# Kernel tuning notes

Measured on AMD Instinct MI355X. Metric: run time of the kernel, lower is better.

Reference implementation:

```python
import jax, jax.numpy as jnp
import numpy as np
import math

# dims (match init_kwargs / input_specs)
T, B, S = 2048, 8, 512
D, H, DFF, NQ, W = 512, 8, 2048, 10, 16
EPS = 1e-5
NEG = -1e30


def _ln(x, g, b):
    mu = jnp.mean(x, axis=-1, keepdims=True)
    var = jnp.mean((x - mu) ** 2, axis=-1, keepdims=True)
    return (x - mu) * jax.lax.rsqrt(var + EPS) * g + b


def setup_inputs() -> dict:
    key = jax.random.key(0)
    ks = jax.random.split(key, 10)
    f = lambda k, shape, s=0.02: jax.random.normal(k, shape, jnp.float32) * s
    return {
        'tgt': jax.random.normal(ks[0], (T, B, D), jnp.float32),
        'memory': jax.random.normal(ks[1], (S, B, D), jnp.float32),
        'queries': f(ks[2], (NQ, D), 1.0 / math.sqrt(D)),
        'wk': f(ks[3], (NQ, 1), 1.0 / math.sqrt(NQ)),
        'in_proj_w': f(ks[4], (3 * D, D)),
        'in_proj_b': jnp.zeros((3 * D,), jnp.float32),
        'out_proj_w': f(ks[5], (D, D)),
        'out_proj_b': jnp.zeros((D,), jnp.float32),
        'lin1_w': f(ks[6], (DFF, D)),
        'lin1_b': jnp.zeros((DFF,), jnp.float32),
        'lin2_w': f(ks[7], (D, DFF)),
        'lin2_b': jnp.zeros((D,), jnp.float32),
        'ln1_g': jnp.ones((D,), jnp.float32), 'ln1_b': jnp.zeros((D,), jnp.float32),
        'ln2_g': jnp.ones((D,), jnp.float32), 'ln2_b': jnp.zeros((D,), jnp.float32),
        'ln3_g': jnp.ones((D,), jnp.float32), 'ln3_b': jnp.zeros((D,), jnp.float32),
    }


def _qa_block(x, queries, wk):
    # x: (T, B, D). Learned queries: per-head unit-norm + depth scale (QaN).
    dh = D // H
    q = queries.reshape(NQ, H, dh)
    q = q / (jnp.linalg.norm(q, axis=-1, keepdims=True) + 1e-6)
    q = (q / math.sqrt(dh)).reshape(NQ, D)
    # LocalAttention(window=W, look_backward=1, look_forward=1, non-causal, autopad)
    # k = v = x; T % W == 0 so autopad is a no-op.
    xb = jnp.transpose(x, (1, 0, 2))                       # (B, T, D)
    nw = T // W
    scale = D ** -0.5                                      # dim_head = D (single-head local attn)
    bk = xb.reshape(B, nw, W, D)
    pad = jnp.zeros((B, 1, W, D), x.dtype)
    bkp = jnp.concatenate([pad, bk, pad], axis=1)          # (B, nw+2, W, D)
    kv = jnp.concatenate([bkp[:, i:i + nw] for i in range(3)], axis=2)  # (B, nw, 3W, D)
    win_ok = jnp.pad(jnp.ones((nw,), bool), (1, 1))
    vm = jnp.stack([win_ok[i:i + nw] for i in range(3)], axis=1)        # (nw, 3)
    kmask = jnp.repeat(vm, W, axis=1)                                   # (nw, 3W)
    # The query vector is identical for every time step, so every position in a
    # window sees the same (query, keyset) pair -> one attention row per (n, window).
    sim = jnp.einsum('nd,bmjd->bnmj', q * scale, kv)       # (B, NQ, nw, 3W)
    sim = jnp.where(kmask[None, None], sim, NEG)
    attn = jax.nn.softmax(sim, axis=-1)
    out = jnp.einsum('bnmj,bmjd->bnmd', attn, kv)          # (B, NQ, nw, D)
    out = jnp.einsum('bnmd,n->bmd', out, wk[:, 0])         # mix N queries via wk (N,1)
    out = jnp.broadcast_to(out[:, :, None], (B, nw, W, D)).reshape(B, T, D)
    return jnp.transpose(out, (1, 0, 2))                   # (T, B, D)


def _mha_block(x, mem, in_w, in_b, out_w, out_b):
    dh = D // H
    wq, wkk, wv = jnp.split(in_w, 3, axis=0)
    bq, bk, bv = jnp.split(in_b, 3)
    q = (x @ wq.T + bq).reshape(T, B, H, dh).transpose(1, 2, 0, 3)   # (B,H,T,dh)
    k = (mem @ wkk.T + bk).reshape(S, B, H, dh).transpose(1, 2, 0, 3)
    v = (mem @ wv.T + bv).reshape(S, B, H, dh).transpose(1, 2, 0, 3)
    attn = jax.nn.softmax(jnp.einsum('bhtd,bhsd->bhts', q, k) / math.sqrt(dh), axis=-1)
    o = jnp.einsum('bhts,bhsd->bhtd', attn, v).transpose(2, 0, 1, 3).reshape(T, B, D)
    return o @ out_w.T + out_b


def reference(tgt, memory, queries, wk, in_proj_w, in_proj_b, out_proj_w, out_proj_b,
              lin1_w, lin1_b, lin2_w, lin2_b, ln1_g, ln1_b, ln2_g, ln2_b, ln3_g, ln3_b):
    # post-norm (norm_first=False), eval mode: dropouts + stochastic_depth(rate=0) are identity
    x = tgt
    x = _ln(x + _qa_block(x, queries, wk), ln1_g, ln1_b)
    x = _ln(x + _mha_block(x, memory, in_proj_w, in_proj_b, out_proj_w, out_proj_b), ln2_g, ln2_b)
    ff = jax.nn.relu(x @ lin1_w.T + lin1_b) @ lin2_w.T + lin2_b
    x = _ln(x + ff, ln3_g, ln3_b)
    # x = tgt + stochastic_depth(x - tgt) == x in eval / rate 0
    return x
```

## Files before the change

kernel.cpp:

```cpp
#include <hip/hip_runtime.h>


typedef unsigned short u16;
typedef unsigned int u32;
typedef short short8_t __attribute__((ext_vector_type(8)));
typedef float f32x4 __attribute__((ext_vector_type(4)));

#define TT 2048
#define BB 8
#define SS 512
#define DD 512
#define HH 8
#define DH 64
#define DFF 2048
#define NQ 10
#define WW 16
#define NW 128
#define KVPART 2097152

__device__ __forceinline__ float b2f(u16 u) {
    return __uint_as_float(((unsigned int)u) << 16);
}
__device__ __forceinline__ u16 f2b(float f) {
    unsigned int x = __float_as_uint(f);
    unsigned int r = x + 0x7FFFu + ((x >> 16) & 1u);
    return (u16)(r >> 16);
}
__device__ __forceinline__ u32 cvt_pk_bf16(float lo, float hi) {
    u32 r;
    asm volatile("v_cvt_pk_bf16_f32 %0, %1, %2" : "=v"(r) : "v"(lo), "v"(hi));
    return r;
}
__device__ __forceinline__ float wave_sum(float v) {
    #pragma unroll
    for (int o = 32; o > 0; o >>= 1) v += __shfl_xor(v, o, 64);
    return v;
}
__device__ __forceinline__ float wave_max(float v) {
    #pragma unroll
    for (int o = 32; o > 0; o >>= 1) v = fmaxf(v, __shfl_xor(v, o, 64));
    return v;
}
__device__ __forceinline__ void load4(const u16* p, float* v) {
    ushort4 t = *(const ushort4*)p;
    v[0] = b2f(t.x); v[1] = b2f(t.y); v[2] = b2f(t.z); v[3] = b2f(t.w);
}
__device__ __forceinline__ void load4(const float* p, float* v) {
    float4 t = *(const float4*)p;
    v[0] = t.x; v[1] = t.y; v[2] = t.z; v[3] = t.w;
}
__device__ __forceinline__ void st1(u16* p, float v) { *p = f2b(v); }
__device__ __forceinline__ void st1(float* p, float v) { *p = v; }

__device__ __forceinline__ void async16(const u16* g, u16* l) {
    __builtin_amdgcn_global_load_lds((const __attribute__((address_space(1))) u32*)g,
                                     (__attribute__((address_space(3))) u32*)l, 16, 0, 0);
}

__device__ __forceinline__ void xcd_remap(int& bx, int& by) {
    int flat = blockIdx.y * gridDim.x + blockIdx.x;
    int xcd = flat & 7;
    int j = flat >> 3;
    by = xcd * ((int)gridDim.y >> 3) + j / (int)gridDim.x;
    bx = j % (int)gridDim.x;
}

__device__ __forceinline__ void cvt_block(const float* s, u16* d, int base) {
    int i = base + threadIdx.x * 4;
    float4 v = *(const float4*)(s + i);
    ushort4 o;
    o.x = f2b(v.x); o.y = f2b(v.y); o.z = f2b(v.z); o.w = f2b(v.w);
    *(ushort4*)(d + i) = o;
}

__global__ __launch_bounds__(256) void cvt2_kernel(const float* __restrict__ s0,
                                                   const float* __restrict__ s1,
                                                   u16* __restrict__ d0,
                                                   u16* __restrict__ d1) {
    int bid = blockIdx.x;
    if (bid < 2048) cvt_block(s0, d0, bid * 1024);
    else            cvt_block(s1, d1, (bid - 2048) * 1024);
}

__global__ __launch_bounds__(256) void cvt3_kernel(const float* __restrict__ s0,
                                                   const float* __restrict__ s1,
                                                   const float* __restrict__ s2,
                                                   u16* __restrict__ d0,
                                                   u16* __restrict__ d1,
                                                   u16* __restrict__ d2) {
    int bid = blockIdx.x;
    if (bid < 256) {
        cvt_block(s0, d0, bid * 1024);
    } else if (bid < 1280) {
        cvt_block(s1, d1, (bid - 256) * 1024);
    } else {
        int g = (bid - 1280) * 256 + threadIdx.x;
        int l = g & 63, ot = (g >> 6) & 31, c = g >> 11;
        int quad = l >> 4;
        int o = ot * 16 + (l & 15);
        const float* src = s2 + (size_t)o * DFF + c * 32 + 4 * quad;
        float4 v0 = *(const float4*)(src);
        float4 v1 = *(const float4*)(src + 16);
        ushort4 o0, o1;
        o0.x = f2b(v0.x); o0.y = f2b(v0.y); o0.z = f2b(v0.z); o0.w = f2b(v0.w);
        o1.x = f2b(v1.x); o1.y = f2b(v1.y); o1.z = f2b(v1.z); o1.w = f2b(v1.w);
        u16* dst = d2 + (size_t)g * 8;
        *(ushort4*)(dst) = o0;
        *(ushort4*)(dst + 4) = o1;
    }
}

__global__ __launch_bounds__(512) void qeff_kernel(const float* __restrict__ queries,
                                                   float* __restrict__ qeff) {
    int d = threadIdx.x;
    const float KS = 0.0055242717280199026f;
    for (int n = 0; n < NQ; n++) {
        float v = queries[n * DD + d];
        float ss = wave_sum(v * v);
        float norm = sqrtf(ss);
        qeff[n * DD + d] = v / (norm + 1e-6f) * KS;
    }
}

__global__ __launch_bounds__(256) void p_kernel(const float* __restrict__ x,
                                                const float* __restrict__ qeff,
                                                float* __restrict__ p) {
    __shared__ float qe[NQ * DD];
    for (int i = threadIdx.x; i < NQ * DD; i += 256) qe[i] = qeff[i];
    __syncthreads();
    int b = blockIdx.x >> 9;
    int t = ((blockIdx.x & 511) << 2) + (threadIdx.x >> 6);
    int lane = threadIdx.x & 63;
    const float* xr = x + ((size_t)t * BB + b) * DD;
    float acc[NQ];
    #pragma unroll
    for (int n = 0; n < NQ; n++) acc[n] = 0.f;
    #pragma unroll
    for (int c = 0; c < 8; c++) {
        int d = c * 64 + lane;
        float xv = xr[d];
        #pragma unroll
        for (int n = 0; n < NQ; n++) acc[n] += xv * qe[n * DD + d];
    }
    #pragma unroll
    for (int n = 0; n < NQ; n++) {
        float s = wave_sum(acc[n]);
        if (lane == 0) p[((size_t)(b * NQ + n)) * TT + t] = s;
    }
}

__global__ __launch_bounds__(256) void winmix_kernel(const float* __restrict__ p,
                                                     const float* __restrict__ wk,
                                                     const float* __restrict__ x,
                                                     float* __restrict__ mixed) {
    __shared__ float As[48];
    int id = blockIdx.x;
    int b = id >> 7, m = id & 127;
    if (threadIdx.x < 64) {
        int j = threadIdx.x;
        int tj = (m - 1) * WW + j;
        bool valid = (j < 48) && (tj >= 0) && (tj < TT);
        float acc = 0.f;
        for (int n = 0; n < NQ; n++) {
            float v = valid ? p[((size_t)(b * NQ + n)) * TT + tj] : -1e30f;
            float mx = wave_max(v);
            float e = valid ? __expf(v - mx) : 0.f;
            float s = wave_sum(e);
            acc += wk[n] * (e / s);
        }
        if (j < 48) As[j] = acc;
    }
    __syncthreads();
    int d0 = threadIdx.x, d1 = threadIdx.x + 256;
    float a0 = 0.f, a1 = 0.f;
    int tb = (m - 1) * WW;
    for (int j = 0; j < 48; j++) {
        int t = tb + j;
        if ((unsigned)t < (unsigned)TT) {
            float aj = As[j];
            const float* xr = x + ((size_t)t * BB + b) * DD;
            a0 += aj * xr[d0];
            a1 += aj * xr[d1];
        }
    }
    mixed[(size_t)id * DD + d0] = a0;
    mixed[(size_t)id * DD + d1] = a1;
}

__global__ __launch_bounds__(256) void ln_qa_kernel(const float* __restrict__ a,
                                                    const float* __restrict__ mixed,
                                                    const float* __restrict__ g,
                                                    const float* __restrict__ bt,
                                                    u16* __restrict__ out) {
    int r = blockIdx.x * 4 + (threadIdx.x >> 6);
    int lane = threadIdx.x & 63;
    int t = r >> 3, b = r & 7;
    const float* ar = a + (size_t)r * DD;
    const float* mr = mixed + ((size_t)(b * NW + (t >> 4))) * DD;
    int d0 = lane * 8;
    float av[8], mv[8], gg[8], bb[8];
    load4(ar + d0, av); load4(ar + d0 + 4, av + 4);
    load4(mr + d0, mv); load4(mr + d0 + 4, mv + 4);
    load4(g + d0, gg);  load4(g + d0 + 4, gg + 4);
    load4(bt + d0, bb); load4(bt + d0 + 4, bb + 4);
    float v[8];
    float s = 0.f, s2 = 0.f;
    #pragma unroll
    for (int u = 0; u < 8; u++) { v[u] = av[u] + mv[u]; s += v[u]; s2 += v[u] * v[u]; }
    s = wave_sum(s); s2 = wave_sum(s2);
    float mu = s * (1.f / DD);
    float var = s2 * (1.f / DD) - mu * mu;
    float rs = rsqrtf(var + 1e-5f);
    #pragma unroll
    for (int u = 0; u < 8; u++) out[(size_t)r * DD + d0 + u] = f2b((v[u] - mu) * rs * gg[u] + bb[u]);
}

template <typename OT>
__global__ __launch_bounds__(256) void ln_rows_kernel(const u16* __restrict__ a,
                                                      const u16* __restrict__ bsrc,
                                                      const float* __restrict__ g,
                                                      const float* __restrict__ bt,
                                                      OT* __restrict__ out) {
    int r = blockIdx.x * 4 + (threadIdx.x >> 6);
    int lane = threadIdx.x & 63;
    const u16* ar = a + (size_t)r * DD;
    const u16* br = bsrc + (size_t)r * DD;
    int d0 = lane * 8;
    float av[8], cv[8], gg[8], bb[8];
    load4(ar + d0, av); load4(ar + d0 + 4, av + 4);
    load4(br + d0, cv); load4(br + d0 + 4, cv + 4);
    load4(g + d0, gg);  load4(g + d0 + 4, gg + 4);
    load4(bt + d0, bb); load4(bt + d0 + 4, bb + 4);
    float v[8];
    float s = 0.f, s2 = 0.f;
    #pragma unroll
    for (int u = 0; u < 8; u++) { v[u] = av[u] + cv[u]; s += v[u]; s2 += v[u] * v[u]; }
    s = wave_sum(s); s2 = wave_sum(s2);
    float mu = s * (1.f / DD);
    float var = s2 * (1.f / DD) - mu * mu;
    float rs = rsqrtf(var + 1e-5f);
    #pragma unroll
    for (int u = 0; u < 8; u++) st1(out + (size_t)r * DD + d0 + u, (v[u] - mu) * rs * gg[u] + bb[u]);
}

template <int RELU, int MT, int KV>
__global__ __launch_bounds__(256) void gemm_lds(const u16* __restrict__ A,
                                                const u16* __restrict__ W,
                                                const float* __restrict__ bias,
                                                u16* __restrict__ C,
                                                int M, int N, int K) {
    constexpr int BM = MT * 32;
    constexpr int NIA = BM / 64;
    __shared__ u16 As[2][BM * 32];
    __shared__ u16 Bs[2][128 * 32];
    int tid = threadIdx.x;
    int w = tid >> 6, lane = tid & 63;
    int n16 = lane & 15, quad = lane >> 4;
    int m0 = blockIdx.y * BM, n0 = blockIdx.x * 128;
    int wm16 = (w >> 1) * MT;
    int wn = (w & 1) * 64;

    const u16* gA[NIA];
    u16* lA[NIA];
    #pragma unroll
    for (int i = 0; i < NIA; i++) {
        int s = (w * NIA + i) * 64 + lane;
        int mb = s >> 6, kseg = (s >> 4) & 3, m = s & 15;
        gA[i] = A + (size_t)(m0 + mb * 16 + m) * K + kseg * 8;
        lA[i] = &As[0][(size_t)((w * NIA + i) * 64) * 8];
    }
    const u16* gB[2];
    u16* lB[2];
    #pragma unroll
    for (int i = 0; i < 2; i++) {
        int s = (w * 2 + i) * 64 + lane;
        int nb = s >> 6, kseg = (s >> 4) & 3, n = s & 15;
        gB[i] = W + (size_t)(n0 + nb * 16 + n) * K + kseg * 8;
        lB[i] = &Bs[0][(size_t)((w * 2 + i) * 64) * 8];
    }

    f32x4 acc[MT][4];
    #pragma unroll
    for (int i = 0; i < MT; i++)
        #pragma unroll
        for (int j = 0; j < 4; j++) acc[i][j] = (f32x4){0.f, 0.f, 0.f, 0.f};

    const int nk = K >> 5;
    #pragma unroll
    for (int i = 0; i < NIA; i++) async16(gA[i], lA[i]);
    #pragma unroll
    for (int i = 0; i < 2; i++) async16(gB[i], lB[i]);
    __syncthreads();

    for (int t = 0; t < nk; t++) {
        int cur = t & 1;
        if (t + 1 < nk) {
            int nxt = cur ^ 1;
            #pragma unroll
            for (int i = 0; i < NIA; i++) async16(gA[i] + (t + 1) * 32, lA[i] + nxt * (BM * 32));
            #pragma unroll
            for (int i = 0; i < 2; i++) async16(gB[i] + (t + 1) * 32, lB[i] + nxt * 4096);
        }
        const u16* Ac = &As[cur][0];
        const u16* Bc = &Bs[cur][0];
        short8_t af[MT], bf[4];
        #pragma unroll
        for (int im = 0; im < MT; im++)
            af[im] = *(const short8_t*)(Ac + (size_t)((wm16 + im) * 64 + lane) * 8);
        #pragma unroll
        for (int in = 0; in < 4; in++)
            bf[in] = *(const short8_t*)(Bc + (size_t)(((w & 1) * 4 + in) * 64 + lane) * 8);
        #pragma unroll
        for (int im = 0; im < MT; im++)
            #pragma unroll
            for (int in = 0; in < 4; in++)
                acc[im][in] = __builtin_amdgcn_mfma_f32_16x16x32_bf16(af[im], bf[in], acc[im][in], 0, 0, 0);
        __syncthreads();
    }

    float bia[4];
    #pragma unroll
    for (int in = 0; in < 4; in++) bia[in] = bias[n0 + wn + in * 16 + n16];
    #pragma unroll
    for (int im = 0; im < MT; im++) {
        #pragma unroll
        for (int r = 0; r < 4; r++) {
            int row = m0 + (wm16 + im) * 16 + quad * 4 + r;
            #pragma unroll
            for (int in = 0; in < 4; in++) {
                float v = acc[im][in][r] + bia[in];
                if (RELU) v = fmaxf(v, 0.f);
                if (KV) {
                    int col = n0 + wn + in * 16 + n16;
                    int part = col >> 9, h = (col >> 6) & 7, d = col & 63;
                    int s = row >> 3, bq = row & 7;
                    C[(size_t)part * KVPART + ((size_t)(bq * HH + h) * SS + s) * DH + d] = f2b(v);
                } else {
                    C[(size_t)row * N + n0 + wn + in * 16 + n16] = f2b(v);
                }
            }
        }
    }
}

template <int RELU, int KV>
__global__ __launch_bounds__(256) void gemm_np(const u16* __restrict__ A,
                                               const u16* __restrict__ W,
                                               const float* __restrict__ bias,
                                               u16* __restrict__ C,
                                               int M, int N, int K) {
    __shared__ u16 As[3][64 * 32];
    __shared__ u16 Bs[3][64 * 32];
    int tid = threadIdx.x;
    int w = tid >> 6, lane = tid & 63;
    int n16 = lane & 15, quad = lane >> 4;
    int bx, by;
    xcd_remap(bx, by);
    int m0 = by * 64, n0 = bx * 64;
    int wm16 = (w >> 1) * 2;
    int wn = (w & 1) * 32;

    const u16* gA0 = A + (size_t)(m0 + w * 16 + n16) * K + quad * 8;
    const u16* gB0 = W + (size_t)(n0 + w * 16 + n16) * K + quad * 8;

    f32x4 acc[2][2];
    #pragma unroll
    for (int i = 0; i < 2; i++)
        #pragma unroll
        for (int j = 0; j < 2; j++) acc[i][j] = (f32x4){0.f, 0.f, 0.f, 0.f};

    const int nk = K >> 5;
    async16(gA0, &As[0][w * 512]);
    async16(gB0, &Bs[0][w * 512]);
    async16(gA0 + 32, &As[1][w * 512]);
    async16(gB0 + 32, &Bs[1][w * 512]);

    int cur = 0;
    for (int t = 0; t < nk; t++) {
        if (t + 1 < nk) {
            __asm__ volatile("s_waitcnt vmcnt(2)" ::: "memory");
        } else {
            __asm__ volatile("s_waitcnt vmcnt(0)" ::: "memory");
        }
        __builtin_amdgcn_s_barrier();
        __builtin_amdgcn_sched_barrier(0);
        if (t + 2 < nk) {
            int nx2 = cur + 2; if (nx2 >= 3) nx2 -= 3;
            async16(gA0 + (t + 2) * 32, &As[nx2][w * 512]);
            async16(gB0 + (t + 2) * 32, &Bs[nx2][w * 512]);
        }
        const u16* Ac = &As[cur][0];
        const u16* Bc = &Bs[cur][0];
        short8_t af[2], bf[2];
        #pragma unroll
        for (int im = 0; im < 2; im++)
            af[im] = *(const short8_t*)(Ac + (size_t)((wm16 + im) * 64 + lane) * 8);
        #pragma unroll
        for (int in = 0; in < 2; in++)
            bf[in] = *(const short8_t*)(Bc + (size_t)(((w & 1) * 2 + in) * 64 + lane) * 8);
        #pragma unroll
        for (int im = 0; im < 2; im++)
            #pragma unroll
            for (int in = 0; in < 2; in++)
                acc[im][in] = __builtin_amdgcn_mfma_f32_16x16x32_bf16(af[im], bf[in], acc[im][in], 0, 0, 0);
        __asm__ volatile("s_waitcnt lgkmcnt(0)" ::: "memory");
        cur = (cur == 2) ? 0 : cur + 1;
    }

    float bia[2];
    #pragma unroll
    for (int in = 0; in < 2; in++) bia[in] = bias[n0 + wn + in * 16 + n16];
    #pragma unroll
    for (int im = 0; im < 2; im++) {
        #pragma unroll
        for (int r = 0; r < 4; r++) {
            int row = m0 + (wm16 + im) * 16 + quad * 4 + r;
            #pragma unroll
            for (int in = 0; in < 2; in++) {
                float v = acc[im][in][r] + bia[in];
                if (RELU) v = fmaxf(v, 0.f);
                if (KV) {
                    int col = n0 + wn + in * 16 + n16;
                    int part = col >> 9, h = (col >> 6) & 7, d = col & 63;
                    int s = row >> 3, bq = row & 7;
                    C[(size_t)part * KVPART + ((size_t)(bq * HH + h) * SS + s) * DH + d] = f2b(v);
                } else {
                    C[(size_t)row * N + n0 + wn + in * 16 + n16] = f2b(v);
                }
            }
        }
    }
}

__global__ __launch_bounds__(256, 1) void ffn_fused(const u16* __restrict__ A,
                                                    const u16* __restrict__ W1,
                                                    const float* __restrict__ b1,
                                                    const u16* __restrict__ W2s,
                                                    const float* __restrict__ b2,
                                                    u16* __restrict__ Cout) {
    __shared__ u16 W1b[2][32 * 512];
    __shared__ float b1s[DFF];
    int tid = threadIdx.x;
    int w = tid >> 6, lane = tid & 63;
    int n16 = lane & 15, quad = lane >> 4, q8 = quad * 8;
    int m0 = blockIdx.x * 64;
    int row = m0 + w * 16 + n16;

    for (int i = tid; i < DFF; i += 256) b1s[i] = b1[i];

    short8_t aq[16];
    {
        const u16* ar = A + (size_t)row * DD + q8;
        #pragma unroll
        for (int ks = 0; ks < 16; ks++)
            aq[ks] = *(const short8_t*)(ar + ks * 32);
    }

    const u16* gW1 = W1 + (size_t)((w >> 1) * 16 + n16) * DD + ((w & 1) * 8) * 32 + q8;
    const u16* gW2 = W2s + lane * 8;

    f32x4 acc[32];
    #pragma unroll
    for (int ot = 0; ot < 32; ot++) acc[ot] = (f32x4){0.f, 0.f, 0.f, 0.f};

    union PU { u32 wd[4]; short8_t s8; };

    #pragma unroll
    for (int i = 0; i < 8; i++)
        async16(gW1 + i * 32, &W1b[0][(size_t)(w * 8 + i) * 512]);
    __syncthreads();

    for (int c = 0; c < 64; c++) {
        int cur = c & 1, nxt = cur ^ 1;

        short8_t w2f[32];
        {
            const u16* gw2c = gW2 + (size_t)c * 16384;
            #pragma unroll
            for (int f = 0; f < 32; f++)
                w2f[f] = *(const short8_t*)(gw2c + f * 512);
        }

        if (c < 63) {
            const u16* gW1c = gW1 + (size_t)(c + 1) * 32 * DD;
            #pragma unroll
            for (int i = 0; i < 8; i++)
                async16(gW1c + i * 32, &W1b[nxt][(size_t)(w * 8 + i) * 512]);
        }

        f32x4 s0 = (f32x4){0.f, 0.f, 0.f, 0.f};
        f32x4 s1 = (f32x4){0.f, 0.f, 0.f, 0.f};
        #pragma unroll
        for (int ks = 0; ks < 16; ks++) {
            short8_t f0 = *(const short8_t*)&W1b[cur][(size_t)ks * 512 + lane * 8];
            s0 = __builtin_amdgcn_mfma_f32_16x16x32_bf16(f0, aq[ks], s0, 0, 0, 0);
        }
        #pragma unroll
        for (int ks = 0; ks < 16; ks++) {
            short8_t f1 = *(const short8_t*)&W1b[cur][(size_t)(16 + ks) * 512 + lane * 8];
            s1 = __builtin_amdgcn_mfma_f32_16x16x32_bf16(f1, aq[ks], s1, 0, 0, 0);
        }

        float p0 = fmaxf(s0[0] + b1s[c * 32 + quad * 4 + 0], 0.f);
        float p1 = fmaxf(s0[1] + b1s[c * 32 + quad * 4 + 1], 0.f);
        float p2 = fmaxf(s0[2] + b1s[c * 32 + quad * 4 + 2], 0.f);
        float p3 = fmaxf(s0[3] + b1s[c * 32 + quad * 4 + 3], 0.f);
        float p4 = fmaxf(s1[0] + b1s[c * 32 + 16 + quad * 4 + 0], 0.f);
        float p5 = fmaxf(s1[1] + b1s[c * 32 + 16 + quad * 4 + 1], 0.f);
        float p6 = fmaxf(s1[2] + b1s[c * 32 + 16 + quad * 4 + 2], 0.f);
        float p7 = fmaxf(s1[3] + b1s[c * 32 + 16 + quad * 4 + 3], 0.f);

        PU pu;
        pu.wd[0] = cvt_pk_bf16(p0, p1);
        pu.wd[1] = cvt_pk_bf16(p2, p3);
        pu.wd[2] = cvt_pk_bf16(p4, p5);
        pu.wd[3] = cvt_pk_bf16(p6, p7);

        #pragma unroll
        for (int ot = 0; ot < 32; ot++)
            acc[ot] = __builtin_amdgcn_mfma_f32_16x16x32_bf16(pu.s8, w2f[ot], acc[ot], 0, 0, 0);

        __syncthreads();
    }

    #pragma unroll
    for (int ot = 0; ot < 32; ot++) {
        float bia = b2[ot * 16 + n16];
        #pragma unroll
        for (int r = 0; r < 4; r++) {
            int ro = m0 + w * 16 + quad * 4 + r;
            Cout[(size_t)ro * DD + ot * 16 + n16] = f2b(acc[ot][r] + bia);
        }
    }
}

__global__ __launch_bounds__(256) void attn_wp(const u16* __restrict__ qb,
                                               const u16* __restrict__ kvb,
                                               u16* __restrict__ ob) {
    __shared__ u16 Kb[2][2048];
    __shared__ u16 Vt[2][64][40];
    int tid = threadIdx.x;
    int w = tid >> 6, lane = tid & 63;
    int n16 = lane & 15, quad = lane >> 4, q8 = quad * 8;
    int xb, bh;
    xcd_remap(xb, bh);
    int b = bh >> 3, h = bh & 7;
    int q0 = xb * 128 + w * 32;

    short8_t aq[2][2];
    #pragma unroll
    for (int qt = 0; qt < 2; qt++) {
        const u16* qrow = qb + ((size_t)(q0 + qt * 16 + n16) * BB + b) * DD + h * DH;
        aq[qt][0] = *(const short8_t*)(qrow + q8);
        aq[qt][1] = *(const short8_t*)(qrow + 32 + q8);
    }

    const u16* kbase = kvb + (size_t)(b * HH + h) * (SS * DH);
    const u16* vbase = kvb + (size_t)KVPART + (size_t)(b * HH + h) * (SS * DH);

    const u16* gK = kbase + (size_t)((w >> 1) * 16 + n16) * DH + (w & 1) * 32 + q8;

    int m = lane & 15;
    int a2 = m >> 2, b2 = m & 3;
    int key0 = (b2 < 2) ? (4 * a2 + 2 * b2) : (16 + 4 * a2 + 2 * (b2 - 2));
    int kp2 = m * 2;
    int vd = w * 16 + quad * 4;
    const u16* gV = vbase + (size_t)key0 * DH + vd;

    float lsum[2] = {0.f, 0.f};
    f32x4 Oa[2][4];
    #pragma unroll
    for (int qt = 0; qt < 2; qt++)
        #pragma unroll
        for (int ot = 0; ot < 4; ot++) Oa[qt][ot] = (f32x4){0.f, 0.f, 0.f, 0.f};

    union VU { ushort4 q; u16 h[4]; };
    union PU { u32 wd[4]; short8_t s8; };

    {
        async16(gK, &Kb[0][w * 512]);
        VU va, vb2;
        va.q  = *(const ushort4*)(gV);
        vb2.q = *(const ushort4*)(gV + DH);
        #pragma unroll
        for (int u = 0; u < 4; u++)
            *(u32*)&Vt[0][vd + u][kp2] = (u32)va.h[u] | ((u32)vb2.h[u] << 16);
    }
    __syncthreads();

    for (int c = 0; c < 16; c++) {
        int cur = c & 1, nxt = cur ^ 1;

        VU va, vb2;
        if (c < 15) {
            const u16* gVc = gV + (size_t)(c + 1) * 32 * DH;
            va.q  = *(const ushort4*)(gVc);
            vb2.q = *(const ushort4*)(gVc + DH);
            async16(gK + (size_t)(c + 1) * 32 * DH, &Kb[nxt][w * 512]);
        }

        short8_t bk0 = *(const short8_t*)&Kb[cur][0 * 512 + lane * 8];
        short8_t bk1 = *(const short8_t*)&Kb[cur][1 * 512 + lane * 8];
        short8_t bk2 = *(const short8_t*)&Kb[cur][2 * 512 + lane * 8];
        short8_t bk3 = *(const short8_t*)&Kb[cur][3 * 512 + lane * 8];

        #pragma unroll
        for (int qt = 0; qt < 2; qt++) {
            f32x4 s0 = (f32x4){0.f, 0.f, 0.f, 0.f};
            s0 = __builtin_amdgcn_mfma_f32_16x16x32_bf16(bk0, aq[qt][0], s0, 0, 0, 0);
            s0 = __builtin_amdgcn_mfma_f32_16x16x32_bf16(bk1, aq[qt][1], s0, 0, 0, 0);
            f32x4 s1 = (f32x4){0.f, 0.f, 0.f, 0.f};
            s1 = __builtin_amdgcn_mfma_f32_16x16x32_bf16(bk2, aq[qt][0], s1, 0, 0, 0);
            s1 = __builtin_amdgcn_mfma_f32_16x16x32_bf16(bk3, aq[qt][1], s1, 0, 0, 0);

            float p0 = __expf(s0[0] * 0.125f - 8.0f);
            float p1 = __expf(s0[1] * 0.125f - 8.0f);
            float p2 = __expf(s0[2] * 0.125f - 8.0f);
            float p3 = __expf(s0[3] * 0.125f - 8.0f);
            float p4 = __expf(s1[0] * 0.125f - 8.0f);
            float p5 = __expf(s1[1] * 0.125f - 8.0f);
            float p6 = __expf(s1[2] * 0.125f - 8.0f);
            float p7 = __expf(s1[3] * 0.125f - 8.0f);
            lsum[qt] += ((p0 + p1) + (p2 + p3)) + ((p4 + p5) + (p6 + p7));

            PU pu;
            pu.wd[0] = cvt_pk_bf16(p0, p1);
            pu.wd[1] = cvt_pk_bf16(p2, p3);
            pu.wd[2] = cvt_pk_bf16(p4, p5);
            pu.wd[3] = cvt_pk_bf16(p6, p7);

            #pragma unroll
            for (int ot = 0; ot < 4; ot++) {
                short8_t bv = *(const short8_t*)&Vt[cur][ot * 16 + n16][q8];
                Oa[qt][ot] = __builtin_amdgcn_mfma_f32_16x16x32_bf16(pu.s8, bv, Oa[qt][ot], 0, 0, 0);
            }
        }

        if (c < 15) {
            #pragma unroll
            for (int u = 0; u < 4; u++)
                *(u32*)&Vt[nxt][vd + u][kp2] = (u32)va.h[u] | ((u32)vb2.h[u] << 16);
        }
        __syncthreads();
    }

    #pragma unroll
    for (int qt = 0; qt < 2; qt++) {
        float l = lsum[qt];
        l += __shfl_xor(l, 16, 64);
        l += __shfl_xor(l, 32, 64);
        #pragma unroll
        for (int r = 0; r < 4; r++) {
            float lq = __shfl(l, quad * 4 + r, 64);
            float inv = 1.f / lq;
            int t = q0 + qt * 16 + quad * 4 + r;
            u16* orow = ob + ((size_t)t * BB + b) * DD + h * DH + n16;
            #pragma unroll
            for (int ot = 0; ot < 4; ot++) orow[ot * 16] = f2b(Oa[qt][ot][r] * inv);
        }
    }
}

extern "C" void kernel_launch(void* const* d_in, const int* in_sizes, int n_in,
                              void* d_out, int out_size, void* d_ws, size_t ws_size,
                              hipStream_t stream) {
    const float* tgt       = (const float*)d_in[0];
    const float* memory    = (const float*)d_in[1];
    const float* queries   = (const float*)d_in[2];
    const float* wk        = (const float*)d_in[3];
    const float* in_proj_w = (const float*)d_in[4];
    const float* in_proj_b = (const float*)d_in[5];
    const float* out_proj_w= (const float*)d_in[6];
    const float* out_proj_b= (const float*)d_in[7];
    const float* lin1_w    = (const float*)d_in[8];
    const float* lin1_b    = (const float*)d_in[9];
    const float* lin2_w    = (const float*)d_in[10];
    const float* lin2_b    = (const float*)d_in[11];
    const float* ln1_g     = (const float*)d_in[12];
    const float* ln1_b     = (const float*)d_in[13];
    const float* ln2_g     = (const float*)d_in[14];
    const float* ln2_b     = (const float*)d_in[15];
    const float* ln3_g     = (const float*)d_in[16];
    const float* ln3_b     = (const float*)d_in[17];

    char* w = (char*)d_ws;
    float* qeff  = (float*)(w + 0);
    float* pbuf  = (float*)(w + 20480);
    float* mixed = (float*)(w + 872448);
    u16* y1  = (u16*)(w + 2969600);
    u16* qb  = (u16*)(w + 19746816);
    u16* kvb = (u16*)(w + 36524032);
    u16* ob  = (u16*)(w + 44912640);
    u16* ipwb = (u16*)(w + 44912640);
    u16* memb = (u16*)(w + 46485504);
    u16* opwb  = (u16*)(w + 36524032);
    u16* l1wb  = (u16*)(w + 37048320);
    u16* l2sig = (u16*)(w + 39145472);
    u16* t1 = qb;
    u16* y2 = ob;
    u16* fb = y1;

    cvt2_kernel<<<2816, 256, 0, stream>>>(memory, in_proj_w, memb, ipwb);

    qeff_kernel<<<1, 512, 0, stream>>>(queries, qeff);
    p_kernel<<<BB * (TT / 4), 256, 0, stream>>>(tgt, qeff, pbuf);
    winmix_kernel<<<BB * NW, 256, 0, stream>>>(pbuf, wk, tgt, mixed);
    ln_qa_kernel<<<(TT * BB) / 4, 256, 0, stream>>>(tgt, mixed, ln1_g, ln1_b, y1);

    gemm_lds<0, 4, 0><<<dim3(DD / 128, (TT * BB) / 128), 256, 0, stream>>>(y1, ipwb, in_proj_b, qb, TT * BB, DD, DD);
    gemm_np<0, 1><<<dim3(1024 / 64, (SS * BB) / 64), 256, 0, stream>>>(memb, ipwb + (size_t)DD * DD, in_proj_b + DD, kvb, SS * BB, 1024, DD);
    attn_wp<<<dim3(TT / 128, BB * HH), 256, 0, stream>>>(qb, kvb, ob);
    cvt3_kernel<<<1792, 256, 0, stream>>>(out_proj_w, lin1_w, lin2_w, opwb, l1wb, l2sig);
    gemm_lds<0, 4, 0><<<dim3(DD / 128, (TT * BB) / 128), 256, 0, stream>>>(ob, opwb, out_proj_b, t1, TT * BB, DD, DD);
    ln_rows_kernel<u16><<<(TT * BB) / 4, 256, 0, stream>>>(y1, t1, ln2_g, ln2_b, y2);

    ffn_fused<<<(TT * BB) / 64, 256, 0, stream>>>(y2, l1wb, lin1_b, l2sig, lin2_b, fb);
    ln_rows_kernel<float><<<(TT * BB) / 4, 256, 0, stream>>>(y2, fb, ln3_g, ln3_b, (float*)d_out);
}
```

Baseline: 474.3 us.

## Split FFN hidden dimension across two wave groups with LDS reduction

The fused FFN kernel moves from 256 to 512 threads per block. Two groups of four waves each take alternating 32-wide chunks of the hidden dimension (split-K over DFF), each with its own double-buffered W1 staging, so every wave runs half as many iterations. At the end the second group writes its fp32 partial accumulators to LDS and the first group adds them before applying the bias and storing. This aims to raise per-CU wave parallelism and hide latency, at the cost of doubled LDS for W1, an extra reduction pass through LDS, and register pressure under the 512-thread, 2-blocks-per-CU launch bound.

```diff
diff --git a/kernel.cpp b/kernel.cpp
--- a/kernel.cpp
+++ b/kernel.cpp
@@ -432,21 +432,22 @@
     }
 }
 
-__global__ __launch_bounds__(256, 1) void ffn_fused(const u16* __restrict__ A,
+__global__ __launch_bounds__(512, 2) void ffn_fused(const u16* __restrict__ A,
                                                     const u16* __restrict__ W1,
                                                     const float* __restrict__ b1,
                                                     const u16* __restrict__ W2s,
                                                     const float* __restrict__ b2,
                                                     u16* __restrict__ Cout) {
-    __shared__ u16 W1b[2][32 * 512];
+    __shared__ u16 W1b[4][32 * 512];
     __shared__ float b1s[DFF];
     int tid = threadIdx.x;
     int w = tid >> 6, lane = tid & 63;
+    int g = w >> 2, wi = w & 3;
     int n16 = lane & 15, quad = lane >> 4, q8 = quad * 8;
     int m0 = blockIdx.x * 64;
-    int row = m0 + w * 16 + n16;
-
-    for (int i = tid; i < DFF; i += 256) b1s[i] = b1[i];
+    int row = m0 + wi * 16 + n16;
+
+    for (int i = tid; i < DFF; i += 512) b1s[i] = b1[i];
 
     short8_t aq[16];
     {
@@ -456,7 +457,7 @@
             aq[ks] = *(const short8_t*)(ar + ks * 32);
     }
 
-    const u16* gW1 = W1 + (size_t)((w >> 1) * 16 + n16) * DD + ((w & 1) * 8) * 32 + q8;
+    const u16* gW1 = W1 + (size_t)((wi >> 1) * 16 + n16) * DD + ((wi & 1) * 8) * 32 + q8;
     const u16* gW2 = W2s + lane * 8;
 
     f32x4 acc[32];
@@ -466,12 +467,13 @@
     union PU { u32 wd[4]; short8_t s8; };
 
     #pragma unroll
-    for (int i = 0; i < 8; i++)
-        async16(gW1 + i * 32, &W1b[0][(size_t)(w * 8 + i) * 512]);
+    for (int k = 0; k < 8; k++)
+        async16(gW1 + (size_t)g * 16384 + k * 32, &W1b[g * 2][(size_t)(wi * 8 + k) * 512]);
     __syncthreads();
 
-    for (int c = 0; c < 64; c++) {
-        int cur = c & 1, nxt = cur ^ 1;
+    for (int i = 0; i < 32; i++) {
+        int c = 2 * i + g;
+        int cur = i & 1, nxt = cur ^ 1;
 
         short8_t w2f[32];
         {
@@ -481,23 +483,24 @@
                 w2f[f] = *(const short8_t*)(gw2c + f * 512);
         }
 
-        if (c < 63) {
-            const u16* gW1c = gW1 + (size_t)(c + 1) * 32 * DD;
-            #pragma unroll
-            for (int i = 0; i < 8; i++)
-                async16(gW1c + i * 32, &W1b[nxt][(size_t)(w * 8 + i) * 512]);
-        }
-
+        if (i < 31) {
+            const u16* gW1c = gW1 + (size_t)(c + 2) * 16384;
+            #pragma unroll
+            for (int k = 0; k < 8; k++)
+                async16(gW1c + k * 32, &W1b[g * 2 + nxt][(size_t)(wi * 8 + k) * 512]);
+        }
+
+        const u16* W1c = &W1b[g * 2 + cur][0];
         f32x4 s0 = (f32x4){0.f, 0.f, 0.f, 0.f};
         f32x4 s1 = (f32x4){0.f, 0.f, 0.f, 0.f};
         #pragma unroll
         for (int ks = 0; ks < 16; ks++) {
-            short8_t f0 = *(const short8_t*)&W1b[cur][(size_t)ks * 512 + lane * 8];
+            short8_t f0 = *(const short8_t*)(W1c + (size_t)ks * 512 + lane * 8);
             s0 = __builtin_amdgcn_mfma_f32_16x16x32_bf16(f0, aq[ks], s0, 0, 0, 0);
         }
         #pragma unroll
         for (int ks = 0; ks < 16; ks++) {
-            short8_t f1 = *(const short8_t*)&W1b[cur][(size_t)(16 + ks) * 512 + lane * 8];
+            short8_t f1 = *(const short8_t*)(W1c + (size_t)(16 + ks) * 512 + lane * 8);
             s1 = __builtin_amdgcn_mfma_f32_16x16x32_bf16(f1, aq[ks], s1, 0, 0, 0);
         }
 
@@ -523,13 +526,27 @@
         __syncthreads();
     }
 
-    #pragma unroll
-    for (int ot = 0; ot < 32; ot++) {
-        float bia = b2[ot * 16 + n16];
-        #pragma unroll
-        for (int r = 0; r < 4; r++) {
-            int ro = m0 + w * 16 + quad * 4 + r;
-            Cout[(size_t)ro * DD + ot * 16 + n16] = f2b(acc[ot][r] + bia);
+    float* red = (float*)&W1b[0][0];
+    if (g == 1) {
+        float* rw = red + (size_t)wi * 8192;
+        #pragma unroll
+        for (int ot = 0; ot < 32; ot++)
+            #pragma unroll
+            for (int r = 0; r < 4; r++)
+                rw[(ot * 4 + r) * 64 + lane] = acc[ot][r];
+    }
+    __syncthreads();
+    if (g == 0) {
+        const float* rw = red + (size_t)wi * 8192;
+        #pragma unroll
+        for (int ot = 0; ot < 32; ot++) {
+            float bia = b2[ot * 16 + n16];
+            #pragma unroll
+            for (int r = 0; r < 4; r++) {
+                float v = acc[ot][r] + rw[(ot * 4 + r) * 64 + lane] + bia;
+                int ro = m0 + wi * 16 + quad * 4 + r;
+                Cout[(size_t)ro * DD + ot * 16 + n16] = f2b(v);
+            }
         }
     }
 }
@@ -714,6 +731,6 @@
     gemm_lds<0, 4, 0><<<dim3(DD / 128, (TT * BB) / 128), 256, 0, stream>>>(ob, opwb, out_proj_b, t1, TT * BB, DD, DD);
     ln_rows_kernel<u16><<<(TT * BB) / 4, 256, 0, stream>>>(y1, t1, ln2_g, ln2_b, y2);
 
-    ffn_fused<<<(TT * BB) / 64, 256, 0, stream>>>(y2, l1wb, lin1_b, l2sig, lin2_b, fb);
+    ffn_fused<<<(TT * BB) / 64, 512, 0, stream>>>(y2, l1wb, lin1_b, l2sig, lin2_b, fb);
     ln_rows_kernel<float><<<(TT * BB) / 4, 256, 0, stream>>>(y2, fb, ln3_g, ln3_b, (float*)d_out);
 }
```

Result: slower. 675.3 us (+42.4%).
